# Performance work log

Measured on AMD Instinct MI355X. Metric: run time of the kernel, lower is better.

Reference implementation:

```python
import jax, jax.numpy as jnp
import numpy as np

P = 5  # patchsize == stride (non-overlapping)


def unfold_patches(x, p):
    # x: [N, C, H, W] -> [N, L, C, p, p], blocks ordered row-major (matches F.unfold)
    N, C, H, W = x.shape
    x = x.reshape(N, C, H // p, p, W // p, p)
    return x.transpose(0, 2, 4, 1, 3, 5).reshape(N, (H // p) * (W // p), C, p, p)


def fold_patches(pat, H, W, p):
    # [N, L, C, p, p] -> [N, C, H, W]; stride==kernel so F.fold is pure placement (no overlap sums)
    N, L, C, _, _ = pat.shape
    x = pat.reshape(N, H // p, W // p, C, p, p)
    return x.transpose(0, 3, 1, 4, 2, 5).reshape(N, C, H, W)


def gather_scale_concat(fold, idx, gamma):
    # fold: [N, L, C, p, p]; idx: [N, L, 4] int; gamma: [4]
    def gath(k):
        return jnp.take_along_axis(fold, idx[:, :, k][:, :, None, None, None], axis=1)
    # first slot uses patch j itself (not idx[...,0]), per the original loop body
    return jnp.concatenate(
        [gamma[0] * fold, gamma[1] * gath(1), gamma[2] * gath(2), gamma[3] * gath(3)], axis=2)


def conv3x3(x, w, b):
    y = jax.lax.conv_general_dilated(x, w, window_strides=(1, 1), padding='SAME',
                                     dimension_numbers=('NCHW', 'OIHW', 'NCHW'))
    return y + b[None, :, None, None]


def setup_inputs() -> dict:
    key = jax.random.key(0)
    ks = jax.random.split(key, 7)
    N, C, H, W = 4, 32, 300, 300
    L = (H // P) * (W // P)
    x_rgb = jax.random.normal(ks[0], (N, C, H, W), dtype=jnp.float32)
    y_hsi = jax.random.normal(ks[1], (N, C, H, W), dtype=jnp.float32)
    corr = jax.random.randint(ks[2], (2, N, L, 4), 0, L)
    rgb_gamma = jnp.ones((4,), jnp.float32)
    hsi_gamma = jnp.ones((4,), jnp.float32)
    rgb_W = jax.random.normal(ks[3], (C, 4 * C, 3, 3), dtype=jnp.float32) * 0.02
    rgb_b = jnp.zeros((C,), jnp.float32)
    hsi_W = jax.random.normal(ks[4], (C, 4 * C, 3, 3), dtype=jnp.float32) * 0.02
    hsi_b = jnp.zeros((C,), jnp.float32)
    return {'x_rgb': x_rgb, 'y_hsi': y_hsi, 'corr': corr,
            'rgb_gamma': rgb_gamma, 'hsi_gamma': hsi_gamma,
            'rgb_W': rgb_W, 'rgb_b': rgb_b, 'hsi_W': hsi_W, 'hsi_b': hsi_b}


def reference(x_rgb, y_hsi, corr, rgb_gamma, hsi_gamma, rgb_W, rgb_b, hsi_W, hsi_b):
    n_feats = x_rgb.shape[1]
    half = n_feats // 2
    H, W = x_rgb.shape[2], x_rgb.shape[3]
    hsi = jnp.concatenate([x_rgb[:, :half], y_hsi[:, :half]], axis=1)      # [N, n_feats, H, W]
    rgb = jnp.concatenate([x_rgb[:, half:n_feats], y_hsi[:, half:n_feats]], axis=1)
    idx = corr[0]  # [N, L, 4]
    # H, W divisible by P -> calc_padding yields zero padding
    fold_rgb = unfold_patches(rgb, P)  # [N, L, C, p, p]
    fold_hsi = unfold_patches(hsi, P)
    patch_rgb = gather_scale_concat(fold_rgb, idx, rgb_gamma)  # [N, L, 4C, p, p]
    patch_hsi = gather_scale_concat(fold_hsi, idx, hsi_gamma)
    img_rgb = fold_patches(patch_rgb, H, W, P)  # [N, 4C, H, W]
    img_hsi = fold_patches(patch_hsi, H, W, P)
    out_rgb = conv3x3(img_rgb, rgb_W, rgb_b) + rgb
    out_hsi = conv3x3(img_hsi, hsi_W, hsi_b) + hsi
    return (out_rgb, out_hsi)
```

## Files before the change

### kernel.cpp

```cpp
#include <hip/hip_runtime.h>

#define HW        90000
#define OUT_HALF  11520000
#define CPLANE    11520000ull
#define WPACK_OFF  46080000ull
#define ZOFF       46227456
#define JB_OFF     46227520
#define WS_NEED    (46227520ull + 230400ull)

typedef short short4v __attribute__((ext_vector_type(4)));
typedef short short8 __attribute__((ext_vector_type(8)));
typedef int   int4v  __attribute__((ext_vector_type(4)));
typedef float f32x4  __attribute__((ext_vector_type(4)));
typedef unsigned int u32;

__device__ inline short f2bf(float f) {
    unsigned u = __builtin_bit_cast(unsigned, f);
    u += 0x7fff + ((u >> 16) & 1);
    return (short)(u >> 16);
}
__device__ inline float bf2f(short s) {
    unsigned u = ((unsigned)(unsigned short)s) << 16;
    return __builtin_bit_cast(float, u);
}
__device__ inline void gload16(char* ldst, const char* gsrc) {
    __builtin_amdgcn_global_load_lds(
        (const __attribute__((address_space(1))) u32*)gsrc,
        (__attribute__((address_space(3))) u32*)ldst, 16, 0, 0);
}

__global__ __launch_bounds__(256)
void pack_weights(const float* __restrict__ wR, const float* __restrict__ wH,
                  const float* __restrict__ rg, const float* __restrict__ hg,
                  short* __restrict__ wpack) {
    int id = blockIdx.x * 256 + threadIdx.x;
    if (id >= 73728) return;
    int e    = id & 7;
    int lane = (id >> 3) & 63;
    int h    = (id >> 9) & 1;
    int t    = (id >> 10) % 9;
    int kb   = ((id >> 10) / 9) & 3;
    int conv = id / 36864;
    int co   = h * 16 + (lane & 15);
    int cin  = kb * 32 + (lane >> 4) * 8 + e;
    const float* w = conv ? wH : wR;
    const float* g = conv ? hg : rg;
    wpack[id] = f2bf(w[(co * 128 + cin) * 9 + t] * g[cin >> 5]);
}

__global__ __launch_bounds__(256)
void pack_jb(const int* __restrict__ corr, int* __restrict__ jb) {
    int id = blockIdx.x * 256 + threadIdx.x;
    if (id >= 57600) return;
    int k = id & 3, j = (id >> 2) % 3600, n = id / 14400;
    int jp = (k == 0) ? j : corr[(n * 3600 + j) * 4 + k];
    jb[id] = ((jp / 60) * 1500 + (jp % 60) * 5) * 64;
}

__global__ __launch_bounds__(256)
void nchw2nhwc(const float* __restrict__ xrgb, const float* __restrict__ yhsi,
               short* __restrict__ cmb) {
    int wave = threadIdx.x >> 6, lane = threadIdx.x & 63;
    if (lane >= 60) return;
    int y = blockIdx.y * 4 + wave;
    int x = blockIdx.x * 60 + lane;
    int n = blockIdx.z;
    const float* xb = xrgb + n * 32 * HW + y * 300 + x;
    const float* yb = yhsi + n * 32 * HW + y * 300 + x;
    size_t pxo = ((size_t)n * HW + y * 300 + x) * 32;
    short* d0 = cmb + pxo;
    short* d1 = cmb + CPLANE + pxo;
    #pragma unroll
    for (int q = 0; q < 4; ++q) {
        short8 v0, v1;
        #pragma unroll
        for (int e = 0; e < 8; ++e) {
            int c = q * 8 + e;
            v0[e] = f2bf((c < 16) ? xb[(16 + c) * HW] : yb[c * HW]);
            v1[e] = f2bf((c < 16) ? xb[c * HW] : yb[(c - 16) * HW]);
        }
        *(short8*)(d0 + q * 8) = v0;
        *(short8*)(d1 + q * 8) = v1;
    }
}

__global__ __launch_bounds__(256, 4)
void conv_mfma(const char* __restrict__ wsbase, const short* __restrict__ wpack,
               const float* __restrict__ bR, const float* __restrict__ bH,
               float* __restrict__ out) {
    __shared__ alignas(16) char lds[2][16384];
    int tile = blockIdx.x;
    int n = blockIdx.y;
    int conv = blockIdx.z;
    int ty = tile / 19, tx = tile - ty * 19;
    int y0 = ty * 12, x0 = tx * 16;
    int tid = threadIdx.x;
    int wave = tid >> 6, lane = tid & 63;

    const short* cmb = (const short*)wsbase + conv * CPLANE + (size_t)n * HW * 32;
    const short* wp  = wpack + conv * 36864;
    int cmb_byte = (int)(conv * (CPLANE * 2)) + n * (HW * 64);
    const int* jbtab = (const int*)(wsbase + JB_OFF);

    int soffB[4][4];
    #pragma unroll
    for (int ji = 0; ji < 4; ++ji) {
        int j4 = wave + ji * 4;
        int off = j4 * 1024 + lane * 16;
        int pxp = off >> 6;
        int pxl = pxp ^ ((pxp >> 2) & 1);
        int cl  = ((off >> 4) & 3) ^ (pxl & 3);
        int cb  = cl * 16;
        #pragma unroll
        for (int k = 0; k < 4; ++k) soffB[ji][k] = ZOFF + cb;
        if (pxl < 252) {
            int hr = pxl / 18, hc = pxl - hr * 18;
            int gy = y0 + hr - 1, gx = x0 + hc - 1;
            if (gy >= 0 && gy < 300 && gx >= 0 && gx < 300) {
                int pr = gy / 5, pc = gx / 5;
                int j  = pr * 60 + pc;
                int intra = (gy - pr * 5) * 300 + (gx - pc * 5);
                int4v jbv = *(const int4v*)(jbtab + (n * 3600 + j) * 4);
                int base = cmb_byte + intra * 64 + cb;
                soffB[ji][0] = base + jbv[0];
                soffB[ji][1] = base + jbv[1];
                soffB[ji][2] = base + jbv[2];
                soffB[ji][3] = base + jbv[3];
            }
        }
    }

    #define STAGE(buf, k)                                                        \
        do {                                                                     \
            _Pragma("unroll")                                                    \
            for (int ji = 0; ji < 4; ++ji) {                                     \
                int j4 = wave + ji * 4;                                          \
                gload16(&lds[buf][j4 * 1024], wsbase + soffB[ji][(k)]);          \
            }                                                                    \
        } while (0)

    int l15 = lane & 15, lh = lane >> 4;
    int wr = wave * 3;

    int boff[3][5];
    #pragma unroll
    for (int dxi = 0; dxi < 3; ++dxi)
        #pragma unroll
        for (int rr = 0; rr < 5; ++rr) {
            int hp = (wr + rr) * 18 + (l15 + dxi);
            boff[dxi][rr] = (hp * 64 + lh * 16) ^ ((hp & 7) << 4);
        }

    STAGE(0, 0);
    __syncthreads();

    f32x4 acc[3][2];
    #pragma unroll
    for (int g = 0; g < 3; ++g)
        #pragma unroll
        for (int h = 0; h < 2; ++h)
            acc[g][h] = (f32x4){0.f, 0.f, 0.f, 0.f};

    #pragma unroll
    for (int kb = 0; kb < 4; ++kb) {
        short8 a[3][3][2];
        #pragma unroll
        for (int dxi = 0; dxi < 3; ++dxi)
            #pragma unroll
            for (int dyi = 0; dyi < 3; ++dyi) {
                int t = dyi * 3 + dxi;
                a[dxi][dyi][0] = *(const short8*)(wp + (((kb * 9 + t) * 2 + 0) * 64 + lane) * 8);
                a[dxi][dyi][1] = *(const short8*)(wp + (((kb * 9 + t) * 2 + 1) * 64 + lane) * 8);
            }
        __builtin_amdgcn_sched_barrier(0);
        if (kb == 0) STAGE(1, 1);
        if (kb == 1) STAGE(0, 2);
        if (kb == 2) STAGE(1, 3);
        __builtin_amdgcn_sched_barrier(0);
        const char* base = lds[kb & 1];
        __builtin_amdgcn_s_setprio(1);
        #pragma unroll
        for (int dxi = 0; dxi < 3; ++dxi) {
            short8 b[5];
            #pragma unroll
            for (int rr = 0; rr < 5; ++rr)
                b[rr] = *(const short8*)(base + boff[dxi][rr]);
            #pragma unroll
            for (int g = 0; g < 3; ++g) {
                #pragma unroll
                for (int dyi = 0; dyi < 3; ++dyi) {
                    acc[g][0] = __builtin_amdgcn_mfma_f32_16x16x32_bf16(a[dxi][dyi][0], b[g + dyi], acc[g][0], 0, 0, 0);
                    acc[g][1] = __builtin_amdgcn_mfma_f32_16x16x32_bf16(a[dxi][dyi][1], b[g + dyi], acc[g][1], 0, 0, 0);
                }
            }
        }
        __builtin_amdgcn_s_setprio(0);
        if (kb < 3) __syncthreads();
    }

    const float* bias = conv ? bH : bR;
    float bia[2][4];
    #pragma unroll
    for (int h = 0; h < 2; ++h)
        #pragma unroll
        for (int reg = 0; reg < 4; ++reg)
            bia[h][reg] = bias[h * 16 + lh * 4 + reg];
    #pragma unroll
    for (int g = 0; g < 3; ++g) {
        int gy = y0 + wr + g;
        int gx = x0 + l15;
        if (gx < 300) {
            int pixo = gy * 300 + gx;
            const short* resp = cmb + (size_t)pixo * 32 + lh * 4;
            #pragma unroll
            for (int h = 0; h < 2; ++h) {
                short4v r = *(const short4v*)(resp + h * 16);
                #pragma unroll
                for (int reg = 0; reg < 4; ++reg) {
                    int co = h * 16 + lh * 4 + reg;
                    out[conv * OUT_HALF + (n * 32 + co) * HW + pixo]
                        = acc[g][h][reg] + bia[h][reg] + bf2f(r[reg]);
                }
            }
        }
    }
    #undef STAGE
}

__global__ __launch_bounds__(256)
void fused_gather_conv(const float* __restrict__ xrgb, const float* __restrict__ yhsi,
                       const int* __restrict__ corr, const float* __restrict__ rgb_gamma,
                       const float* __restrict__ hsi_gamma, const float* __restrict__ wR,
                       const float* __restrict__ bR, const float* __restrict__ wH,
                       const float* __restrict__ bH, float* __restrict__ out) {
    int tid = blockIdx.x * blockDim.x + threadIdx.x;
    if (tid >= 4 * HW) return;
    int n = tid / HW, pix = tid - n * HW;
    int y = pix / 300, x = pix - y * 300;
    const int* idx = corr + n * (3600 * 4);
    const float* xb = xrgb + n * (32 * HW);
    const float* yb = yhsi + n * (32 * HW);
    float accR[32], accH[32];
    #pragma unroll
    for (int i = 0; i < 32; ++i) { accR[i] = 0.f; accH[i] = 0.f; }
    for (int k = 0; k < 4; ++k) {
        float gr = rgb_gamma[k], gh = hsi_gamma[k];
        int off[9];
        #pragma unroll
        for (int t = 0; t < 9; ++t) {
            int dy = t / 3 - 1, dx = t % 3 - 1;
            int yy = y + dy, xx = x + dx;
            int o = -1;
            if (yy >= 0 && yy < 300 && xx >= 0 && xx < 300) {
                int pr = yy / 5, pc = xx / 5;
                int j = pr * 60 + pc;
                int jp = (k == 0) ? j : idx[j * 4 + k];
                o = ((jp / 60) * 5 + (yy - pr * 5)) * 300 + (jp % 60) * 5 + (xx - pc * 5);
            }
            off[t] = o;
        }
        for (int c = 0; c < 32; ++c) {
            const float* srcR = (c < 16) ? (xb + (16 + c) * HW) : (yb + c * HW);
            const float* srcH = (c < 16) ? (xb + c * HW) : (yb + (c - 16) * HW);
            float vr[9], vh[9];
            #pragma unroll
            for (int t = 0; t < 9; ++t) {
                bool vld = off[t] >= 0;
                vr[t] = vld ? gr * srcR[off[t]] : 0.f;
                vh[t] = vld ? gh * srcH[off[t]] : 0.f;
            }
            const float* wRp = wR + (k * 32 + c) * 9;
            const float* wHp = wH + (k * 32 + c) * 9;
            #pragma unroll
            for (int t = 0; t < 9; ++t)
                #pragma unroll
                for (int co = 0; co < 32; ++co) {
                    accR[co] = fmaf(vr[t], wRp[co * 1152 + t], accR[co]);
                    accH[co] = fmaf(vh[t], wHp[co * 1152 + t], accH[co]);
                }
        }
    }
    #pragma unroll
    for (int co = 0; co < 32; ++co) {
        float resR = (co < 16) ? xb[(16 + co) * HW + pix] : yb[co * HW + pix];
        float resH = (co < 16) ? xb[co * HW + pix] : yb[(co - 16) * HW + pix];
        out[(n * 32 + co) * HW + pix]            = accR[co] + bR[co] + resR;
        out[OUT_HALF + (n * 32 + co) * HW + pix] = accH[co] + bH[co] + resH;
    }
}

extern "C" void kernel_launch(void* const* d_in, const int* in_sizes, int n_in,
                              void* d_out, int out_size, void* d_ws, size_t ws_size,
                              hipStream_t stream) {
    const float* xrgb = (const float*)d_in[0];
    const float* yhsi = (const float*)d_in[1];
    const int*   corr = (const int*)d_in[2];
    const float* rg   = (const float*)d_in[3];
    const float* hg   = (const float*)d_in[4];
    const float* wR   = (const float*)d_in[5];
    const float* bR   = (const float*)d_in[6];
    const float* wH   = (const float*)d_in[7];
    const float* bH   = (const float*)d_in[8];
    float* out = (float*)d_out;

    if (ws_size >= WS_NEED) {
        char* ws = (char*)d_ws;
        hipMemsetAsync(ws + ZOFF, 0, 64, stream);
        hipLaunchKernelGGL(pack_weights, dim3(288), dim3(256), 0, stream,
                           wR, wH, rg, hg, (short*)(ws + WPACK_OFF));
        hipLaunchKernelGGL(pack_jb, dim3(225), dim3(256), 0, stream,
                           corr, (int*)(ws + JB_OFF));
        hipLaunchKernelGGL(nchw2nhwc, dim3(5, 75, 4), dim3(256), 0, stream,
                           xrgb, yhsi, (short*)ws);
        hipLaunchKernelGGL(conv_mfma, dim3(475, 4, 2), dim3(256), 0, stream,
                           (const char*)ws, (const short*)(ws + WPACK_OFF), bR, bH, out);
    } else {
        int total = 4 * HW;
        hipLaunchKernelGGL(fused_gather_conv, dim3((total + 255) / 256), dim3(256), 0, stream,
                           xrgb, yhsi, corr, rg, hg, wR, bR, wH, bH, out);
    }
}
```

Baseline: 136.4 us.

## Stage all four K-blocks into LDS at once and drop double-buffer syncs

Replaces the two-buffer LDS pipeline (four staged K-blocks with a barrier between each) with a single 63 KB LDS tile that holds all four gathered K-blocks, loaded up front behind one barrier. The LDS layout becomes 256 bytes per pixel with an XOR swizzle, and the K-block is selected by XOR on the address. Weight fragments are now loaded per dx inside the loop, which lowers register pressure. Occupancy drops from 4 to 2 blocks per CU because of the larger LDS footprint. Global loads no longer overlap with MFMA work inside a block, so latency hiding now depends on the other resident block.

```diff
diff --git a/kernel.cpp b/kernel.cpp
--- a/kernel.cpp
+++ b/kernel.cpp
@@ -84,11 +84,11 @@
     }
 }
 
-__global__ __launch_bounds__(256, 4)
+__global__ __launch_bounds__(256, 2)
 void conv_mfma(const char* __restrict__ wsbase, const short* __restrict__ wpack,
                const float* __restrict__ bR, const float* __restrict__ bH,
                float* __restrict__ out) {
-    __shared__ alignas(16) char lds[2][16384];
+    __shared__ alignas(16) char lds[64512];
     int tile = blockIdx.x;
     int n = blockIdx.y;
     int conv = blockIdx.z;
@@ -102,56 +102,46 @@
     int cmb_byte = (int)(conv * (CPLANE * 2)) + n * (HW * 64);
     const int* jbtab = (const int*)(wsbase + JB_OFF);
 
-    int soffB[4][4];
-    #pragma unroll
-    for (int ji = 0; ji < 4; ++ji) {
+    int soff[16];
+    #pragma unroll
+    for (int ji = 0; ji < 16; ++ji) {
         int j4 = wave + ji * 4;
-        int off = j4 * 1024 + lane * 16;
-        int pxp = off >> 6;
-        int pxl = pxp ^ ((pxp >> 2) & 1);
-        int cl  = ((off >> 4) & 3) ^ (pxl & 3);
-        int cb  = cl * 16;
-        #pragma unroll
-        for (int k = 0; k < 4; ++k) soffB[ji][k] = ZOFF + cb;
-        if (pxl < 252) {
-            int hr = pxl / 18, hc = pxl - hr * 18;
+        int px = j4 * 4 + (lane >> 4);
+        int un = ((lane & 15) << 4) ^ ((px & 7) << 4);
+        int k  = (un >> 6) & 3;
+        int chunk = un & 48;
+        soff[ji] = ZOFF + chunk;
+        if (j4 < 63) {
+            int hr = px / 18, hc = px - hr * 18;
             int gy = y0 + hr - 1, gx = x0 + hc - 1;
             if (gy >= 0 && gy < 300 && gx >= 0 && gx < 300) {
                 int pr = gy / 5, pc = gx / 5;
                 int j  = pr * 60 + pc;
                 int intra = (gy - pr * 5) * 300 + (gx - pc * 5);
-                int4v jbv = *(const int4v*)(jbtab + (n * 3600 + j) * 4);
-                int base = cmb_byte + intra * 64 + cb;
-                soffB[ji][0] = base + jbv[0];
-                soffB[ji][1] = base + jbv[1];
-                soffB[ji][2] = base + jbv[2];
-                soffB[ji][3] = base + jbv[3];
-            }
-        }
-    }
-
-    #define STAGE(buf, k)                                                        \
-        do {                                                                     \
-            _Pragma("unroll")                                                    \
-            for (int ji = 0; ji < 4; ++ji) {                                     \
-                int j4 = wave + ji * 4;                                          \
-                gload16(&lds[buf][j4 * 1024], wsbase + soffB[ji][(k)]);          \
-            }                                                                    \
-        } while (0)
+                soff[ji] = cmb_byte + jbtab[(n * 3600 + j) * 4 + k] + intra * 64 + chunk;
+            }
+        }
+    }
+
+    #pragma unroll
+    for (int ji = 0; ji < 16; ++ji) {
+        int j4 = wave + ji * 4;
+        if (j4 < 63)
+            gload16(&lds[j4 * 1024], wsbase + soff[ji]);
+    }
 
     int l15 = lane & 15, lh = lane >> 4;
     int wr = wave * 3;
 
-    int boff[3][5];
+    int boff0[3][5];
     #pragma unroll
     for (int dxi = 0; dxi < 3; ++dxi)
         #pragma unroll
         for (int rr = 0; rr < 5; ++rr) {
             int hp = (wr + rr) * 18 + (l15 + dxi);
-            boff[dxi][rr] = (hp * 64 + lh * 16) ^ ((hp & 7) << 4);
-        }
-
-    STAGE(0, 0);
+            boff0[dxi][rr] = (hp * 256 + lh * 16) ^ ((hp & 7) << 4);
+        }
+
     __syncthreads();
 
     f32x4 acc[3][2];
@@ -161,42 +151,33 @@
         for (int h = 0; h < 2; ++h)
             acc[g][h] = (f32x4){0.f, 0.f, 0.f, 0.f};
 
+    __builtin_amdgcn_s_setprio(1);
     #pragma unroll
     for (int kb = 0; kb < 4; ++kb) {
-        short8 a[3][3][2];
-        #pragma unroll
-        for (int dxi = 0; dxi < 3; ++dxi)
+        #pragma unroll
+        for (int dxi = 0; dxi < 3; ++dxi) {
+            short8 a[3][2];
             #pragma unroll
             for (int dyi = 0; dyi < 3; ++dyi) {
                 int t = dyi * 3 + dxi;
-                a[dxi][dyi][0] = *(const short8*)(wp + (((kb * 9 + t) * 2 + 0) * 64 + lane) * 8);
-                a[dxi][dyi][1] = *(const short8*)(wp + (((kb * 9 + t) * 2 + 1) * 64 + lane) * 8);
-            }
-        __builtin_amdgcn_sched_barrier(0);
-        if (kb == 0) STAGE(1, 1);
-        if (kb == 1) STAGE(0, 2);
-        if (kb == 2) STAGE(1, 3);
-        __builtin_amdgcn_sched_barrier(0);
-        const char* base = lds[kb & 1];
-        __builtin_amdgcn_s_setprio(1);
-        #pragma unroll
-        for (int dxi = 0; dxi < 3; ++dxi) {
+                a[dyi][0] = *(const short8*)(wp + (((kb * 9 + t) * 2 + 0) * 64 + lane) * 8);
+                a[dyi][1] = *(const short8*)(wp + (((kb * 9 + t) * 2 + 1) * 64 + lane) * 8);
+            }
             short8 b[5];
             #pragma unroll
             for (int rr = 0; rr < 5; ++rr)
-                b[rr] = *(const short8*)(base + boff[dxi][rr]);
+                b[rr] = *(const short8*)(lds + (boff0[dxi][rr] ^ (kb << 6)));
             #pragma unroll
             for (int g = 0; g < 3; ++g) {
                 #pragma unroll
                 for (int dyi = 0; dyi < 3; ++dyi) {
-                    acc[g][0] = __builtin_amdgcn_mfma_f32_16x16x32_bf16(a[dxi][dyi][0], b[g + dyi], acc[g][0], 0, 0, 0);
-                    acc[g][1] = __builtin_amdgcn_mfma_f32_16x16x32_bf16(a[dxi][dyi][1], b[g + dyi], acc[g][1], 0, 0, 0);
+                    acc[g][0] = __builtin_amdgcn_mfma_f32_16x16x32_bf16(a[dyi][0], b[g + dyi], acc[g][0], 0, 0, 0);
+                    acc[g][1] = __builtin_amdgcn_mfma_f32_16x16x32_bf16(a[dyi][1], b[g + dyi], acc[g][1], 0, 0, 0);
                 }
             }
         }
-        __builtin_amdgcn_s_setprio(0);
-        if (kb < 3) __syncthreads();
-    }
+    }
+    __builtin_amdgcn_s_setprio(0);
 
     const float* bias = conv ? bH : bR;
     float bia[2][4];
@@ -224,7 +205,6 @@
             }
         }
     }
-    #undef STAGE
 }
 
 __global__ __launch_bounds__(256)
```

New measurement: 164.6 us. +20.6%, slower.
